# Optimization experiments

Measured on AMD Instinct MI355X. Metric: run time of the kernel, lower is better.

The kernel has to match this reference:

```python
import jax, jax.numpy as jnp
import numpy as np

B, T, L_CTX = 64, 150, 256
H = 512   # decoder_num_hidden
E = 512   # target_embedding_size
V = 1000  # target_vocab_size


def setup_inputs() -> dict:
    key = jax.random.key(0)
    ks = jax.random.split(key, 10)
    s = 0.05
    return {
        "cnn_feats": jax.random.normal(ks[0], (B, L_CTX, H), dtype=jnp.float32),
        "seq": jax.random.randint(ks[1], (B, T), 0, V, dtype=jnp.int32),
        "embed_table": jax.random.normal(ks[2], (V, E), dtype=jnp.float32) * s,
        "W_ih": jax.random.normal(ks[3], (4 * H, E), dtype=jnp.float32) * s,
        "b_ih": jnp.zeros((4 * H,), dtype=jnp.float32),
        "W_hh": jax.random.normal(ks[4], (4 * H, H), dtype=jnp.float32) * s,
        "b_hh": jnp.zeros((4 * H,), dtype=jnp.float32),
        "W_hm": jax.random.normal(ks[5], (H, H), dtype=jnp.float32) * s,
        "W_om": jax.random.normal(ks[6], (H, 2 * H), dtype=jnp.float32) * s,
        "W_logit": jax.random.normal(ks[7], (V, H), dtype=jnp.float32) * s,
        "b_logit": jnp.zeros((V,), dtype=jnp.float32),
    }


def reference(cnn_feats, seq, embed_table, W_ih, b_ih, W_hh, b_hh,
              W_hm, W_om, W_logit, b_logit):
    # Single-layer LSTMCell decoder with per-step attention (eval mode, dropout=0).
    def step(carry, it):
        h, c = carry                      # [B,H] each
        xt = jax.nn.relu(embed_table[it])  # [B,E]
        gates = xt @ W_ih.T + b_ih + h @ W_hh.T + b_hh  # [B,4H]
        i, f, g, o = jnp.split(gates, 4, axis=1)
        c2 = jax.nn.sigmoid(f) * c + jax.nn.sigmoid(i) * jnp.tanh(g)
        h2 = jax.nn.sigmoid(o) * jnp.tanh(c2)
        mapped = h2 @ W_hm.T              # [B,H]
        attn = jnp.einsum("blh,bh->bl", cnn_feats, mapped)
        w = jax.nn.softmax(attn, axis=1)
        ctx = jnp.einsum("bl,blh->bh", w, cnn_feats)
        out = jnp.concatenate([ctx, h2], axis=1) @ W_om.T  # [B,H]
        logp = jax.nn.log_softmax(out @ W_logit.T + b_logit, axis=1)
        return (h2, c2), logp

    bsz = cnn_feats.shape[0]
    h0 = jnp.zeros((bsz, W_hh.shape[1]), dtype=cnn_feats.dtype)
    c0 = jnp.zeros_like(h0)
    _, outs = jax.lax.scan(step, (h0, c0), seq.T)  # outs: [T,B,V]
    return outs.transpose(1, 0, 2)  # [B,T,V]
```

## Files before the change

### kernel.cpp

```cpp
#include <hip/hip_runtime.h>
#include <math.h>

#define B_  64
#define T_  150
#define L_  256
#define H_  512
#define E_  512
#define V_  1000
#define G4_ 2048
#define DB_ 16
#define HCB 32

typedef _Float16 f16;
typedef f16   f16x8 __attribute__((ext_vector_type(8)));
typedef f16   f16x4 __attribute__((ext_vector_type(4)));
typedef float f32x4 __attribute__((ext_vector_type(4)));
typedef unsigned long long ull;

__device__ __forceinline__ float sigmf(float x) { return 1.0f / (1.0f + expf(-x)); }

__global__ __launch_bounds__(512) void decoder_mfma(
    const int*   __restrict__ seq,
    const float* __restrict__ G,
    const float* __restrict__ Whh,
    ull*  __restrict__ xh,
    int*  __restrict__ tags,
    float* __restrict__ hbuf)
{
    __shared__ f16   hlds[64][520];
    __shared__ float glds[64][132];
    __shared__ float csh[64][36];

    const int tid = threadIdx.x;
    const int bb  = blockIdx.x;
    const int ln  = tid & 63;
    const int wv  = tid >> 6;
    const int mh  = wv >> 2;
    const int nt2 = wv & 3;

    f16x8 bfr[2][16];
    #pragma unroll
    for (int j = 0; j < 2; ++j) {
        const int n = 2 * nt2 + j;
        const int grow = (n >> 1) * H_ + bb * HCB + (n & 1) * 16 + (ln & 15);
        #pragma unroll
        for (int kt = 0; kt < 16; ++kt) {
            const int k0 = kt * 32 + (ln >> 4) * 8;
            float4 w0 = *(const float4*)(Whh + (size_t)grow * H_ + k0);
            float4 w1 = *(const float4*)(Whh + (size_t)grow * H_ + k0 + 4);
            bfr[j][kt] = (f16x8){(f16)w0.x, (f16)w0.y, (f16)w0.z, (f16)w0.w,
                                 (f16)w1.x, (f16)w1.y, (f16)w1.z, (f16)w1.w};
        }
    }
    for (int e = tid; e < 64 * 520 / 4; e += 512) ((ull*)hlds)[e] = 0ull;
    for (int e = tid; e < 64 * 36; e += 512) ((float*)csh)[e] = 0.f;
    __syncthreads();

    const int cb = tid >> 3, cg = tid & 7;

    for (int t = 0; t < T_; ++t) {
        const int v = seq[cb * T_ + t];
        const float* gp = G + (size_t)v * G4_ + bb * HCB + cg * 4;
        float4 gq0 = *(const float4*)(gp);
        float4 gq1 = *(const float4*)(gp + H_);
        float4 gq2 = *(const float4*)(gp + 2 * H_);
        float4 gq3 = *(const float4*)(gp + 3 * H_);

        if (t > 0) {
            if (tid < DB_) {
                while (__hip_atomic_load(&tags[tid], __ATOMIC_RELAXED,
                                         __HIP_MEMORY_SCOPE_AGENT) < t) {}
            }
            __syncthreads();
            const ull* src = xh + (size_t)(t & 1) * 64 * 128;
            ull v0[8], v1[8];
            #pragma unroll
            for (int it = 0; it < 8; ++it) {
                const int e = tid + it * 512;
                const int b = e >> 6, s = e & 63;
                v0[it] = __hip_atomic_load(&src[b * 128 + 2 * s], __ATOMIC_RELAXED,
                                           __HIP_MEMORY_SCOPE_AGENT);
                v1[it] = __hip_atomic_load(&src[b * 128 + 2 * s + 1], __ATOMIC_RELAXED,
                                           __HIP_MEMORY_SCOPE_AGENT);
            }
            #pragma unroll
            for (int it = 0; it < 8; ++it) {
                const int e = tid + it * 512;
                const int b = e >> 6, s = e & 63;
                ull* dst = (ull*)&hlds[b][s * 8];
                dst[0] = v0[it]; dst[1] = v1[it];
            }
            __syncthreads();
        }

        f32x4 acc00 = {0.f,0.f,0.f,0.f}, acc01 = {0.f,0.f,0.f,0.f};
        f32x4 acc10 = {0.f,0.f,0.f,0.f}, acc11 = {0.f,0.f,0.f,0.f};
        #pragma unroll
        for (int kt = 0; kt < 16; ++kt) {
            const int ko = kt * 32 + (ln >> 4) * 8;
            f16x8 a0 = *(const f16x8*)&hlds[(2 * mh)     * 16 + (ln & 15)][ko];
            f16x8 a1 = *(const f16x8*)&hlds[(2 * mh + 1) * 16 + (ln & 15)][ko];
            acc00 = __builtin_amdgcn_mfma_f32_16x16x32_f16(a0, bfr[0][kt], acc00, 0, 0, 0);
            acc01 = __builtin_amdgcn_mfma_f32_16x16x32_f16(a0, bfr[1][kt], acc01, 0, 0, 0);
            acc10 = __builtin_amdgcn_mfma_f32_16x16x32_f16(a1, bfr[0][kt], acc10, 0, 0, 0);
            acc11 = __builtin_amdgcn_mfma_f32_16x16x32_f16(a1, bfr[1][kt], acc11, 0, 0, 0);
        }
        {
            const int r0 = (2 * mh) * 16 + (ln >> 4) * 4;
            const int r1 = (2 * mh + 1) * 16 + (ln >> 4) * 4;
            const int c0 = (2 * nt2) * 16 + (ln & 15);
            const int c1 = (2 * nt2 + 1) * 16 + (ln & 15);
            #pragma unroll
            for (int i = 0; i < 4; ++i) {
                glds[r0 + i][c0] = acc00[i];
                glds[r0 + i][c1] = acc01[i];
                glds[r1 + i][c0] = acc10[i];
                glds[r1 + i][c1] = acc11[i];
            }
        }
        __syncthreads();

        {
            float4 Gi = *(const float4*)&glds[cb][cg * 4];
            float4 Gf = *(const float4*)&glds[cb][32 + cg * 4];
            float4 Gg = *(const float4*)&glds[cb][64 + cg * 4];
            float4 Go = *(const float4*)&glds[cb][96 + cg * 4];
            float4 cold = *(const float4*)&csh[cb][cg * 4];
            float gi[4] = {Gi.x + gq0.x, Gi.y + gq0.y, Gi.z + gq0.z, Gi.w + gq0.w};
            float gf[4] = {Gf.x + gq1.x, Gf.y + gq1.y, Gf.z + gq1.z, Gf.w + gq1.w};
            float gg[4] = {Gg.x + gq2.x, Gg.y + gq2.y, Gg.z + gq2.z, Gg.w + gq2.w};
            float go[4] = {Go.x + gq3.x, Go.y + gq3.y, Go.z + gq3.z, Go.w + gq3.w};
            float cl[4] = {cold.x, cold.y, cold.z, cold.w};
            float4 cnew, hnew;
            f16x4 hp;
            #pragma unroll
            for (int i = 0; i < 4; ++i) {
                float c2 = sigmf(gf[i]) * cl[i] + sigmf(gi[i]) * tanhf(gg[i]);
                float h2 = sigmf(go[i]) * tanhf(c2);
                ((float*)&cnew)[i] = c2;
                ((float*)&hnew)[i] = h2;
                hp[i] = (f16)h2;
            }
            *(float4*)&csh[cb][cg * 4] = cnew;
            *(float4*)&hbuf[((size_t)t * 64 + cb) * H_ + bb * HCB + cg * 4] = hnew;
            __hip_atomic_store(
                &xh[(size_t)((t + 1) & 1) * 64 * 128 + cb * 128 + bb * 8 + cg],
                __builtin_bit_cast(ull, hp),
                __ATOMIC_RELAXED, __HIP_MEMORY_SCOPE_AGENT);
        }
        __syncthreads();
        if (tid == 0)
            __hip_atomic_store(&tags[bb], t + 1, __ATOMIC_RELAXED,
                               __HIP_MEMORY_SCOPE_AGENT);
    }
}

template<bool RELU_A, bool REMAP>
__global__ __launch_bounds__(256) void gemm16_nt(
    const float* __restrict__ A1, const float* __restrict__ A2,
    const float* __restrict__ Bm,
    const float* __restrict__ bias1, const float* __restrict__ bias2,
    float* __restrict__ C, int M, int N, int KA)
{
    __shared__ f16 As[64][40];
    __shared__ f16 Bs[64][40];
    const int tid = threadIdx.x;
    const int m0 = blockIdx.x * 64, n0 = blockIdx.y * 64;
    const int ln = tid & 63, wv = tid >> 6;
    const int lr = tid >> 2, lc8 = (tid & 3) * 8;
    const int K = A2 ? 2 * KA : KA;
    f32x4 acc[4] = {};

    for (int kb = 0; kb < K; kb += 32) {
        const float* Ap; int kk;
        if (kb < KA) { Ap = A1; kk = kb; } else { Ap = A2; kk = kb - KA; }
        int gm = m0 + lr;
        float4 a0 = make_float4(0.f, 0.f, 0.f, 0.f), a1 = a0;
        if (gm < M) {
            a0 = *(const float4*)(Ap + (size_t)gm * KA + kk + lc8);
            a1 = *(const float4*)(Ap + (size_t)gm * KA + kk + lc8 + 4);
        }
        if (RELU_A) {
            a0.x = fmaxf(a0.x, 0.f); a0.y = fmaxf(a0.y, 0.f);
            a0.z = fmaxf(a0.z, 0.f); a0.w = fmaxf(a0.w, 0.f);
            a1.x = fmaxf(a1.x, 0.f); a1.y = fmaxf(a1.y, 0.f);
            a1.z = fmaxf(a1.z, 0.f); a1.w = fmaxf(a1.w, 0.f);
        }
        f16x8 av = {(f16)a0.x, (f16)a0.y, (f16)a0.z, (f16)a0.w,
                    (f16)a1.x, (f16)a1.y, (f16)a1.z, (f16)a1.w};
        *(f16x8*)&As[lr][lc8] = av;

        int gn = n0 + lr;
        float4 b0 = make_float4(0.f, 0.f, 0.f, 0.f), b1 = b0;
        if (gn < N) {
            b0 = *(const float4*)(Bm + (size_t)gn * K + kb + lc8);
            b1 = *(const float4*)(Bm + (size_t)gn * K + kb + lc8 + 4);
        }
        f16x8 bv = {(f16)b0.x, (f16)b0.y, (f16)b0.z, (f16)b0.w,
                    (f16)b1.x, (f16)b1.y, (f16)b1.z, (f16)b1.w};
        *(f16x8*)&Bs[lr][lc8] = bv;
        __syncthreads();

        f16x8 af = *(const f16x8*)&As[wv * 16 + (ln & 15)][(ln >> 4) * 8];
        #pragma unroll
        for (int ntt = 0; ntt < 4; ++ntt) {
            f16x8 bf = *(const f16x8*)&Bs[ntt * 16 + (ln & 15)][(ln >> 4) * 8];
            acc[ntt] = __builtin_amdgcn_mfma_f32_16x16x32_f16(af, bf, acc[ntt], 0, 0, 0);
        }
        __syncthreads();
    }

    #pragma unroll
    for (int ntt = 0; ntt < 4; ++ntt)
        #pragma unroll
        for (int i = 0; i < 4; ++i) {
            int gm = m0 + wv * 16 + (ln >> 4) * 4 + i;
            int gn = n0 + ntt * 16 + (ln & 15);
            if (gm < M && gn < N) {
                float v = acc[ntt][i];
                if (bias1) v += bias1[gn];
                if (bias2) v += bias2[gn];
                size_t row = REMAP ? ((size_t)(gm & 63) * T_ + (gm >> 6)) : (size_t)gm;
                C[row * (size_t)N + gn] = v;
            }
        }
}

__global__ __launch_bounds__(512) void score_softmax(
    const float* __restrict__ mapped,
    const float* __restrict__ cnn,
    f16* __restrict__ attP)
{
    __shared__ f16   As[64][40];
    __shared__ f16   Bs[256][40];
    __shared__ float sl[64][260];

    const int tid = threadIdx.x;
    const int m0  = blockIdx.x * 64;
    const int b   = blockIdx.y;
    const int ln  = tid & 63, wv = tid >> 6;
    const int mh  = wv >> 2, nq = wv & 3;
    const int ln15 = ln & 15, ln4 = (ln >> 4) * 8;
    const float* cnnb = cnn + (size_t)b * L_ * H_;

    f32x4 acc[2][4] = {};

    for (int kb = 0; kb < H_; kb += 32) {
        {
            int lr = tid >> 3, lc4 = (tid & 7) * 4;
            int t = m0 + lr;
            float4 a = make_float4(0.f, 0.f, 0.f, 0.f);
            if (t < T_) a = *(const float4*)(mapped + ((size_t)t * 64 + b) * H_ + kb + lc4);
            As[lr][lc4 + 0] = (f16)a.x; As[lr][lc4 + 1] = (f16)a.y;
            As[lr][lc4 + 2] = (f16)a.z; As[lr][lc4 + 3] = (f16)a.w;
        }
        {
            int br = tid >> 1, bc16 = (tid & 1) * 16;
            const float* src = cnnb + (size_t)br * H_ + kb + bc16;
            float4 w0 = *(const float4*)(src);
            float4 w1 = *(const float4*)(src + 4);
            float4 w2 = *(const float4*)(src + 8);
            float4 w3 = *(const float4*)(src + 12);
            f16x8 p0 = {(f16)w0.x, (f16)w0.y, (f16)w0.z, (f16)w0.w,
                        (f16)w1.x, (f16)w1.y, (f16)w1.z, (f16)w1.w};
            f16x8 p1 = {(f16)w2.x, (f16)w2.y, (f16)w2.z, (f16)w2.w,
                        (f16)w3.x, (f16)w3.y, (f16)w3.z, (f16)w3.w};
            *(f16x8*)&Bs[br][bc16]     = p0;
            *(f16x8*)&Bs[br][bc16 + 8] = p1;
        }
        __syncthreads();

        f16x8 a0 = *(const f16x8*)&As[(2 * mh)     * 16 + ln15][ln4];
        f16x8 a1 = *(const f16x8*)&As[(2 * mh + 1) * 16 + ln15][ln4];
        #pragma unroll
        for (int nj = 0; nj < 4; ++nj) {
            f16x8 bf = *(const f16x8*)&Bs[(nq * 4 + nj) * 16 + ln15][ln4];
            acc[0][nj] = __builtin_amdgcn_mfma_f32_16x16x32_f16(a0, bf, acc[0][nj], 0, 0, 0);
            acc[1][nj] = __builtin_amdgcn_mfma_f32_16x16x32_f16(a1, bf, acc[1][nj], 0, 0, 0);
        }
        __syncthreads();
    }

    #pragma unroll
    for (int mi = 0; mi < 2; ++mi)
        #pragma unroll
        for (int nj = 0; nj < 4; ++nj)
            #pragma unroll
            for (int i = 0; i < 4; ++i)
                sl[(2 * mh + mi) * 16 + (ln >> 4) * 4 + i][(nq * 4 + nj) * 16 + ln15]
                    = acc[mi][nj][i];
    __syncthreads();

    #pragma unroll
    for (int rr = 0; rr < 8; ++rr) {
        int r = wv * 8 + rr;
        int t = m0 + r;
        if (t < T_) {
            float4 v = *(const float4*)&sl[r][ln * 4];
            float mx = fmaxf(fmaxf(v.x, v.y), fmaxf(v.z, v.w));
            #pragma unroll
            for (int off = 32; off; off >>= 1) mx = fmaxf(mx, __shfl_xor(mx, off));
            float e0 = expf(v.x - mx), e1 = expf(v.y - mx);
            float e2 = expf(v.z - mx), e3 = expf(v.w - mx);
            float s = e0 + e1 + e2 + e3;
            #pragma unroll
            for (int off = 32; off; off >>= 1) s += __shfl_xor(s, off);
            float inv = 1.f / s;
            f16x4 p = {(f16)(e0 * inv), (f16)(e1 * inv), (f16)(e2 * inv), (f16)(e3 * inv)};
            *(f16x4*)(attP + ((size_t)b * T_ + t) * L_ + ln * 4) = p;
        }
    }
}

__global__ __launch_bounds__(256) void ctx16_nn(
    const f16* __restrict__ attP,
    const float* __restrict__ cnn,
    float* __restrict__ ctxout)
{
    __shared__ f16 As[64][40];
    __shared__ f16 Bs[64][40];
    const int tid = threadIdx.x;
    const int m0 = blockIdx.x * 64, n0 = blockIdx.y * 64;
    const int b  = blockIdx.z;
    const int ln = tid & 63, wv = tid >> 6;
    const int ln15 = ln & 15, ln4 = (ln >> 4) * 8;
    const float* cnnb = cnn + (size_t)b * L_ * H_;
    const f16*   pb   = attP + (size_t)b * T_ * L_;
    f32x4 acc[4] = {};

    for (int kb = 0; kb < L_; kb += 32) {
        {
            int lr = tid >> 2, lc8 = (tid & 3) * 8;
            int t = m0 + lr;
            f16x8 av = {};
            if (t < T_) av = *(const f16x8*)(pb + (size_t)t * L_ + kb + lc8);
            *(f16x8*)&As[lr][lc8] = av;
        }
        {
            int br = tid >> 3;
            int nc = (tid & 7) * 8;
            const float* src = cnnb + (size_t)(kb + br) * H_ + n0 + nc;
            float4 w0 = *(const float4*)(src);
            float4 w1 = *(const float4*)(src + 4);
            float wv8[8] = {w0.x, w0.y, w0.z, w0.w, w1.x, w1.y, w1.z, w1.w};
            #pragma unroll
            for (int j = 0; j < 8; ++j) Bs[nc + j][br] = (f16)wv8[j];
        }
        __syncthreads();

        f16x8 af = *(const f16x8*)&As[wv * 16 + ln15][ln4];
        #pragma unroll
        for (int ntt = 0; ntt < 4; ++ntt) {
            f16x8 bf = *(const f16x8*)&Bs[ntt * 16 + ln15][ln4];
            acc[ntt] = __builtin_amdgcn_mfma_f32_16x16x32_f16(af, bf, acc[ntt], 0, 0, 0);
        }
        __syncthreads();
    }

    #pragma unroll
    for (int ntt = 0; ntt < 4; ++ntt)
        #pragma unroll
        for (int i = 0; i < 4; ++i) {
            int t  = m0 + wv * 16 + (ln >> 4) * 4 + i;
            int gn = n0 + ntt * 16 + ln15;
            if (t < T_)
                ctxout[(size_t)b * H_ + (size_t)t * (B_ * H_) + gn] = acc[ntt][i];
        }
}

__global__ __launch_bounds__(256) void logsoftmax_k(float* __restrict__ out)
{
    const int row = blockIdx.x;
    float* p = out + (size_t)row * V_;
    const int tid = threadIdx.x, lane = tid & 63, wave = tid >> 6;
    __shared__ float red[8];

    float vals[4];
    int n = 0;
    float mx = -INFINITY;
    for (int v = tid; v < V_; v += 256) { vals[n] = p[v]; mx = fmaxf(mx, vals[n]); ++n; }
    #pragma unroll
    for (int off = 32; off; off >>= 1) mx = fmaxf(mx, __shfl_xor(mx, off));
    if (lane == 0) red[wave] = mx;
    __syncthreads();
    mx = fmaxf(fmaxf(red[0], red[1]), fmaxf(red[2], red[3]));

    float s = 0.f;
    for (int i = 0; i < n; ++i) s += expf(vals[i] - mx);
    #pragma unroll
    for (int off = 32; off; off >>= 1) s += __shfl_xor(s, off);
    if (lane == 0) red[4 + wave] = s;
    __syncthreads();
    s = red[4] + red[5] + red[6] + red[7];

    const float lse = mx + logf(s);
    n = 0;
    for (int v = tid; v < V_; v += 256) { p[v] = vals[n] - lse; ++n; }
}

extern "C" void kernel_launch(void* const* d_in, const int* in_sizes, int n_in,
                              void* d_out, int out_size, void* d_ws, size_t ws_size,
                              hipStream_t stream)
{
    const float* cnn     = (const float*)d_in[0];
    const int*   seq     = (const int*)d_in[1];
    const float* embed   = (const float*)d_in[2];
    const float* W_ih    = (const float*)d_in[3];
    const float* b_ih    = (const float*)d_in[4];
    const float* W_hh    = (const float*)d_in[5];
    const float* b_hh    = (const float*)d_in[6];
    const float* W_hm    = (const float*)d_in[7];
    const float* W_om    = (const float*)d_in[8];
    const float* W_logit = (const float*)d_in[9];
    const float* b_logit = (const float*)d_in[10];
    float* out = (float*)d_out;

    float* ws = (float*)d_ws;
    float* G    = ws;
    float* hbuf = G + (size_t)V_ * G4_;
    float* outv = hbuf + (size_t)B_ * T_ * H_;
    ull*   xh   = (ull*)(outv + (size_t)B_ * T_ * H_);
    int*   tags = (int*)(xh + 2 * 64 * 128);
    float* mapped = out;
    f16*   attP   = (f16*)(out + (size_t)B_ * T_ * H_);

    hipMemsetAsync(tags, 0, DB_ * sizeof(int), stream);

    gemm16_nt<true, false><<<dim3(16, 32), 256, 0, stream>>>(
        embed, nullptr, W_ih, b_ih, b_hh, G, V_, G4_, E_);

    decoder_mfma<<<DB_, 512, 0, stream>>>(seq, G, W_hh, xh, tags, hbuf);

    gemm16_nt<false, false><<<dim3(150, 8), 256, 0, stream>>>(
        hbuf, nullptr, W_hm, nullptr, nullptr, mapped, B_ * T_, H_, H_);
    score_softmax<<<dim3(3, 64), 512, 0, stream>>>(mapped, cnn, attP);
    ctx16_nn<<<dim3(3, 8, 64), 256, 0, stream>>>(attP, cnn, mapped);
    gemm16_nt<false, false><<<dim3(150, 8), 256, 0, stream>>>(
        mapped, hbuf, W_om, nullptr, nullptr, outv, B_ * T_, H_, H_);
    gemm16_nt<false, true><<<dim3(150, 16), 256, 0, stream>>>(
        outv, nullptr, W_logit, b_logit, nullptr, out, B_ * T_, V_, H_);
    logsoftmax_k<<<B_ * T_, 256, 0, stream>>>(out);
}
```

Baseline: 1.021 ms.

## Fuse decoder and attention/output stages into one persistent megakernel overlapping recurrence

```diff
diff --git a/kernel.cpp b/kernel.cpp
--- a/kernel.cpp
+++ b/kernel.cpp
@@ -9,6 +9,7 @@
 #define V_  1000
 #define G4_ 2048
 #define DB_ 16
+#define NW_ 240
 #define HCB 32
 
 typedef _Float16 f16;
@@ -19,148 +20,448 @@
 
 __device__ __forceinline__ float sigmf(float x) { return 1.0f / (1.0f + expf(-x)); }
 
-__global__ __launch_bounds__(512) void decoder_mfma(
+__device__ __forceinline__ ull aload(const ull* p)
+{
+    return __hip_atomic_load(p, __ATOMIC_RELAXED, __HIP_MEMORY_SCOPE_AGENT);
+}
+
+__global__ __launch_bounds__(512) void mega_decoder(
     const int*   __restrict__ seq,
     const float* __restrict__ G,
     const float* __restrict__ Whh,
-    ull*  __restrict__ xh,
+    const float* __restrict__ cnn,
+    const float* __restrict__ Whm,
+    const float* __restrict__ Wom,
+    const float* __restrict__ Wlg,
+    const float* __restrict__ b_logit,
+    ull*  __restrict__ xhist,
     int*  __restrict__ tags,
-    float* __restrict__ hbuf)
+    int*  __restrict__ wflags,
+    f16*  __restrict__ stageA,
+    f16*  __restrict__ attP,
+    f16*  __restrict__ outv16,
+    float* __restrict__ out)
 {
-    __shared__ f16   hlds[64][520];
-    __shared__ float glds[64][132];
-    __shared__ float csh[64][36];
+    __shared__ __align__(16) char smem[109568];
 
     const int tid = threadIdx.x;
-    const int bb  = blockIdx.x;
+    const int bx  = blockIdx.x;
     const int ln  = tid & 63;
     const int wv  = tid >> 6;
-    const int mh  = wv >> 2;
-    const int nt2 = wv & 3;
-
-    f16x8 bfr[2][16];
-    #pragma unroll
-    for (int j = 0; j < 2; ++j) {
-        const int n = 2 * nt2 + j;
-        const int grow = (n >> 1) * H_ + bb * HCB + (n & 1) * 16 + (ln & 15);
+
+    if (bx < DB_) {
+        f16   (*hlds)[520] = (f16(*)[520])smem;
+        float (*glds)[132] = (float(*)[132])(smem + 66560);
+        float (*csh)[36]   = (float(*)[36])(smem + 100352);
+        const int bb  = bx;
+        const int mh  = wv >> 2;
+        const int nt2 = wv & 3;
+
+        f16x8 bfr[2][16];
         #pragma unroll
-        for (int kt = 0; kt < 16; ++kt) {
-            const int k0 = kt * 32 + (ln >> 4) * 8;
-            float4 w0 = *(const float4*)(Whh + (size_t)grow * H_ + k0);
-            float4 w1 = *(const float4*)(Whh + (size_t)grow * H_ + k0 + 4);
-            bfr[j][kt] = (f16x8){(f16)w0.x, (f16)w0.y, (f16)w0.z, (f16)w0.w,
-                                 (f16)w1.x, (f16)w1.y, (f16)w1.z, (f16)w1.w};
-        }
+        for (int j = 0; j < 2; ++j) {
+            const int n = 2 * nt2 + j;
+            const int grow = (n >> 1) * H_ + bb * HCB + (n & 1) * 16 + (ln & 15);
+            #pragma unroll
+            for (int kt = 0; kt < 16; ++kt) {
+                const int k0 = kt * 32 + (ln >> 4) * 8;
+                float4 w0 = *(const float4*)(Whh + (size_t)grow * H_ + k0);
+                float4 w1 = *(const float4*)(Whh + (size_t)grow * H_ + k0 + 4);
+                bfr[j][kt] = (f16x8){(f16)w0.x, (f16)w0.y, (f16)w0.z, (f16)w0.w,
+                                     (f16)w1.x, (f16)w1.y, (f16)w1.z, (f16)w1.w};
+            }
+        }
+        for (int e = tid; e < 64 * 520 / 4; e += 512) ((ull*)hlds)[e] = 0ull;
+        for (int e = tid; e < 64 * 36; e += 512) ((float*)csh)[e] = 0.f;
+        __syncthreads();
+
+        const int cb = tid >> 3, cg = tid & 7;
+
+        for (int t = 0; t < T_; ++t) {
+            const int v = seq[cb * T_ + t];
+            const float* gp = G + (size_t)v * G4_ + bb * HCB + cg * 4;
+            float4 gq0 = *(const float4*)(gp);
+            float4 gq1 = *(const float4*)(gp + H_);
+            float4 gq2 = *(const float4*)(gp + 2 * H_);
+            float4 gq3 = *(const float4*)(gp + 3 * H_);
+
+            if (t > 0) {
+                if (tid < DB_) {
+                    while (__hip_atomic_load(&tags[tid], __ATOMIC_RELAXED,
+                                             __HIP_MEMORY_SCOPE_AGENT) < t) {}
+                }
+                __syncthreads();
+                const ull* src = xhist + (size_t)t * 8192;
+                ull v0[8], v1[8];
+                #pragma unroll
+                for (int it = 0; it < 8; ++it) {
+                    const int e = tid + it * 512;
+                    const int b = e >> 6, s = e & 63;
+                    v0[it] = aload(&src[b * 128 + 2 * s]);
+                    v1[it] = aload(&src[b * 128 + 2 * s + 1]);
+                }
+                #pragma unroll
+                for (int it = 0; it < 8; ++it) {
+                    const int e = tid + it * 512;
+                    const int b = e >> 6, s = e & 63;
+                    ull* dst = (ull*)&hlds[b][s * 8];
+                    dst[0] = v0[it]; dst[1] = v1[it];
+                }
+                __syncthreads();
+            }
+
+            f32x4 acc00 = {0.f,0.f,0.f,0.f}, acc01 = {0.f,0.f,0.f,0.f};
+            f32x4 acc10 = {0.f,0.f,0.f,0.f}, acc11 = {0.f,0.f,0.f,0.f};
+            #pragma unroll
+            for (int kt = 0; kt < 16; ++kt) {
+                const int ko = kt * 32 + (ln >> 4) * 8;
+                f16x8 a0 = *(const f16x8*)&hlds[(2 * mh)     * 16 + (ln & 15)][ko];
+                f16x8 a1 = *(const f16x8*)&hlds[(2 * mh + 1) * 16 + (ln & 15)][ko];
+                acc00 = __builtin_amdgcn_mfma_f32_16x16x32_f16(a0, bfr[0][kt], acc00, 0, 0, 0);
+                acc01 = __builtin_amdgcn_mfma_f32_16x16x32_f16(a0, bfr[1][kt], acc01, 0, 0, 0);
+                acc10 = __builtin_amdgcn_mfma_f32_16x16x32_f16(a1, bfr[0][kt], acc10, 0, 0, 0);
+                acc11 = __builtin_amdgcn_mfma_f32_16x16x32_f16(a1, bfr[1][kt], acc11, 0, 0, 0);
+            }
+            {
+                const int r0 = (2 * mh) * 16 + (ln >> 4) * 4;
+                const int r1 = (2 * mh + 1) * 16 + (ln >> 4) * 4;
+                const int c0 = (2 * nt2) * 16 + (ln & 15);
+                const int c1 = (2 * nt2 + 1) * 16 + (ln & 15);
+                #pragma unroll
+                for (int i = 0; i < 4; ++i) {
+                    glds[r0 + i][c0] = acc00[i];
+                    glds[r0 + i][c1] = acc01[i];
+                    glds[r1 + i][c0] = acc10[i];
+                    glds[r1 + i][c1] = acc11[i];
+                }
+            }
+            __syncthreads();
+
+            {
+                float4 Gi = *(const float4*)&glds[cb][cg * 4];
+                float4 Gf = *(const float4*)&glds[cb][32 + cg * 4];
+                float4 Gg = *(const float4*)&glds[cb][64 + cg * 4];
+                float4 Go = *(const float4*)&glds[cb][96 + cg * 4];
+                float4 cold = *(const float4*)&csh[cb][cg * 4];
+                float gi[4] = {Gi.x + gq0.x, Gi.y + gq0.y, Gi.z + gq0.z, Gi.w + gq0.w};
+                float gf[4] = {Gf.x + gq1.x, Gf.y + gq1.y, Gf.z + gq1.z, Gf.w + gq1.w};
+                float gg[4] = {Gg.x + gq2.x, Gg.y + gq2.y, Gg.z + gq2.z, Gg.w + gq2.w};
+                float go[4] = {Go.x + gq3.x, Go.y + gq3.y, Go.z + gq3.z, Go.w + gq3.w};
+                float cl[4] = {cold.x, cold.y, cold.z, cold.w};
+                float4 cnew;
+                f16x4 hp;
+                #pragma unroll
+                for (int i = 0; i < 4; ++i) {
+                    float c2 = sigmf(gf[i]) * cl[i] + sigmf(gi[i]) * tanhf(gg[i]);
+                    float h2 = sigmf(go[i]) * tanhf(c2);
+                    ((float*)&cnew)[i] = c2;
+                    hp[i] = (f16)h2;
+                }
+                *(float4*)&csh[cb][cg * 4] = cnew;
+                __hip_atomic_store(
+                    &xhist[(size_t)(t + 1) * 8192 + cb * 128 + bb * 8 + cg],
+                    __builtin_bit_cast(ull, hp),
+                    __ATOMIC_RELAXED, __HIP_MEMORY_SCOPE_AGENT);
+            }
+            __syncthreads();
+            if (tid == 0)
+                __hip_atomic_store(&tags[bb], t + 1, __ATOMIC_RELAXED,
+                                   __HIP_MEMORY_SCOPE_AGENT);
+        }
+        return;
     }
-    for (int e = tid; e < 64 * 520 / 4; e += 512) ((ull*)hlds)[e] = 0ull;
-    for (int e = tid; e < 64 * 36; e += 512) ((float*)csh)[e] = 0.f;
-    __syncthreads();
-
-    const int cb = tid >> 3, cg = tid & 7;
-
-    for (int t = 0; t < T_; ++t) {
-        const int v = seq[cb * T_ + t];
-        const float* gp = G + (size_t)v * G4_ + bb * HCB + cg * 4;
-        float4 gq0 = *(const float4*)(gp);
-        float4 gq1 = *(const float4*)(gp + H_);
-        float4 gq2 = *(const float4*)(gp + 2 * H_);
-        float4 gq3 = *(const float4*)(gp + 3 * H_);
-
-        if (t > 0) {
-            if (tid < DB_) {
+
+    const int wid = bx - DB_;
+    f16   (*As)[40]  = (f16(*)[40])smem;
+    f16   (*Bs)[40]  = (f16(*)[40])(smem + 5120);
+    float (*sl)[260] = (float(*)[260])(smem + 25600);
+    const int ln15 = ln & 15;
+    const int lnk8 = (ln >> 4) * 8;
+    const int lr4  = (ln >> 4) * 4;
+    int epoch = 0;
+
+    auto wbar = [&](int ep) {
+        __syncthreads();
+        if (tid == 0) {
+            __threadfence();
+            __hip_atomic_store(&wflags[wid], ep, __ATOMIC_RELAXED,
+                               __HIP_MEMORY_SCOPE_AGENT);
+        }
+        for (int i = tid; i < NW_; i += 512)
+            while (__hip_atomic_load(&wflags[i], __ATOMIC_RELAXED,
+                                     __HIP_MEMORY_SCOPE_AGENT) < ep)
+                __builtin_amdgcn_s_sleep(1);
+        __syncthreads();
+        if (tid == 0) __threadfence();
+        __syncthreads();
+    };
+
+    for (int c = 0; c < 3; ++c) {
+        const int t0 = c * 64;
+        const int t1 = (t0 + 64 < T_) ? t0 + 64 : T_;
+        if (t1 < T_) {
+            if (tid == 0)
+                while (__hip_atomic_load(&tags[0], __ATOMIC_RELAXED,
+                                         __HIP_MEMORY_SCOPE_AGENT) < t1 + 1)
+                    __builtin_amdgcn_s_sleep(127);
+        } else {
+            if (tid < DB_)
                 while (__hip_atomic_load(&tags[tid], __ATOMIC_RELAXED,
-                                         __HIP_MEMORY_SCOPE_AGENT) < t) {}
-            }
+                                         __HIP_MEMORY_SCOPE_AGENT) < T_)
+                    __builtin_amdgcn_s_sleep(127);
+        }
+        __syncthreads();
+
+        for (int job = wid; job < 512; job += NW_) {
+            const int t = t0 + (job >> 3);
+            if (t >= t1) continue;
+            const int n0 = (job & 7) * 64;
+            f32x4 acc0 = {0.f,0.f,0.f,0.f}, acc1 = {0.f,0.f,0.f,0.f};
+            const int mh = wv >> 2, nt = wv & 3;
+            for (int kb = 0; kb < 512; kb += 32) {
+                {
+                    int b = tid >> 3, s = tid & 7;
+                    ull v = aload(&xhist[(size_t)(t + 1) * 8192 + b * 128 + kb / 4 + s]);
+                    *(ull*)&As[b][s * 4] = v;
+                }
+                {
+                    int n = tid >> 3, s = tid & 7;
+                    float4 w = *(const float4*)(Whm + (size_t)(n0 + n) * 512 + kb + s * 4);
+                    f16x4 p = {(f16)w.x, (f16)w.y, (f16)w.z, (f16)w.w};
+                    *(f16x4*)&Bs[n][s * 4] = p;
+                }
+                __syncthreads();
+                f16x8 a0 = *(const f16x8*)&As[(2 * mh) * 16 + ln15][lnk8];
+                f16x8 a1 = *(const f16x8*)&As[(2 * mh + 1) * 16 + ln15][lnk8];
+                f16x8 bf = *(const f16x8*)&Bs[nt * 16 + ln15][lnk8];
+                acc0 = __builtin_amdgcn_mfma_f32_16x16x32_f16(a0, bf, acc0, 0, 0, 0);
+                acc1 = __builtin_amdgcn_mfma_f32_16x16x32_f16(a1, bf, acc1, 0, 0, 0);
+                __syncthreads();
+            }
+            #pragma unroll
+            for (int i = 0; i < 4; ++i) {
+                int b0r = (2 * mh) * 16 + lr4 + i, b1r = (2 * mh + 1) * 16 + lr4 + i;
+                int n = n0 + nt * 16 + ln15;
+                stageA[((size_t)t * 64 + b0r) * 512 + n] = (f16)acc0[i];
+                stageA[((size_t)t * 64 + b1r) * 512 + n] = (f16)acc1[i];
+            }
+        }
+        wbar(++epoch);
+
+        for (int b = wid; b < 64; b += NW_) {
+            const float* cnnb = cnn + (size_t)b * L_ * H_;
+            const int mh = wv >> 2, nq = wv & 3;
+            f32x4 acc[2][4] = {};
+            for (int kb = 0; kb < H_; kb += 32) {
+                {
+                    int tp = tid >> 3, s = tid & 7;
+                    ull v = 0ull;
+                    if (t0 + tp < t1)
+                        v = *(const ull*)(stageA + ((size_t)(t0 + tp) * 64 + b) * 512 + kb + s * 4);
+                    *(ull*)&As[tp][s * 4] = v;
+                }
+                {
+                    int br = tid >> 1, bc16 = (tid & 1) * 16;
+                    const float* src = cnnb + (size_t)br * H_ + kb + bc16;
+                    float4 w0 = *(const float4*)(src);
+                    float4 w1 = *(const float4*)(src + 4);
+                    float4 w2 = *(const float4*)(src + 8);
+                    float4 w3 = *(const float4*)(src + 12);
+                    f16x8 p0 = {(f16)w0.x, (f16)w0.y, (f16)w0.z, (f16)w0.w,
+                                (f16)w1.x, (f16)w1.y, (f16)w1.z, (f16)w1.w};
+                    f16x8 p1 = {(f16)w2.x, (f16)w2.y, (f16)w2.z, (f16)w2.w,
+                                (f16)w3.x, (f16)w3.y, (f16)w3.z, (f16)w3.w};
+                    *(f16x8*)&Bs[br][bc16]     = p0;
+                    *(f16x8*)&Bs[br][bc16 + 8] = p1;
+                }
+                __syncthreads();
+                f16x8 a0 = *(const f16x8*)&As[(2 * mh) * 16 + ln15][lnk8];
+                f16x8 a1 = *(const f16x8*)&As[(2 * mh + 1) * 16 + ln15][lnk8];
+                #pragma unroll
+                for (int nj = 0; nj < 4; ++nj) {
+                    f16x8 bf = *(const f16x8*)&Bs[(nq * 4 + nj) * 16 + ln15][lnk8];
+                    acc[0][nj] = __builtin_amdgcn_mfma_f32_16x16x32_f16(a0, bf, acc[0][nj], 0, 0, 0);
+                    acc[1][nj] = __builtin_amdgcn_mfma_f32_16x16x32_f16(a1, bf, acc[1][nj], 0, 0, 0);
+                }
+                __syncthreads();
+            }
+            #pragma unroll
+            for (int mi = 0; mi < 2; ++mi)
+                #pragma unroll
+                for (int nj = 0; nj < 4; ++nj)
+                    #pragma unroll
+                    for (int i = 0; i < 4; ++i)
+                        sl[(2 * mh + mi) * 16 + lr4 + i][(nq * 4 + nj) * 16 + ln15]
+                            = acc[mi][nj][i];
             __syncthreads();
-            const ull* src = xh + (size_t)(t & 1) * 64 * 128;
-            ull v0[8], v1[8];
-            #pragma unroll
-            for (int it = 0; it < 8; ++it) {
-                const int e = tid + it * 512;
-                const int b = e >> 6, s = e & 63;
-                v0[it] = __hip_atomic_load(&src[b * 128 + 2 * s], __ATOMIC_RELAXED,
-                                           __HIP_MEMORY_SCOPE_AGENT);
-                v1[it] = __hip_atomic_load(&src[b * 128 + 2 * s + 1], __ATOMIC_RELAXED,
-                                           __HIP_MEMORY_SCOPE_AGENT);
-            }
-            #pragma unroll
-            for (int it = 0; it < 8; ++it) {
-                const int e = tid + it * 512;
-                const int b = e >> 6, s = e & 63;
-                ull* dst = (ull*)&hlds[b][s * 8];
-                dst[0] = v0[it]; dst[1] = v1[it];
+            #pragma unroll
+            for (int rr = 0; rr < 8; ++rr) {
+                int r = wv * 8 + rr;
+                int t = t0 + r;
+                if (t < t1) {
+                    float4 v = *(const float4*)&sl[r][ln * 4];
+                    float mx = fmaxf(fmaxf(v.x, v.y), fmaxf(v.z, v.w));
+                    #pragma unroll
+                    for (int off = 32; off; off >>= 1) mx = fmaxf(mx, __shfl_xor(mx, off));
+                    float e0 = expf(v.x - mx), e1 = expf(v.y - mx);
+                    float e2 = expf(v.z - mx), e3 = expf(v.w - mx);
+                    float s = e0 + e1 + e2 + e3;
+                    #pragma unroll
+                    for (int off = 32; off; off >>= 1) s += __shfl_xor(s, off);
+                    float inv = 1.f / s;
+                    f16x4 p = {(f16)(e0 * inv), (f16)(e1 * inv),
+                               (f16)(e2 * inv), (f16)(e3 * inv)};
+                    *(f16x4*)(attP + ((size_t)b * T_ + t) * L_ + ln * 4) = p;
+                }
             }
             __syncthreads();
         }
-
-        f32x4 acc00 = {0.f,0.f,0.f,0.f}, acc01 = {0.f,0.f,0.f,0.f};
-        f32x4 acc10 = {0.f,0.f,0.f,0.f}, acc11 = {0.f,0.f,0.f,0.f};
-        #pragma unroll
-        for (int kt = 0; kt < 16; ++kt) {
-            const int ko = kt * 32 + (ln >> 4) * 8;
-            f16x8 a0 = *(const f16x8*)&hlds[(2 * mh)     * 16 + (ln & 15)][ko];
-            f16x8 a1 = *(const f16x8*)&hlds[(2 * mh + 1) * 16 + (ln & 15)][ko];
-            acc00 = __builtin_amdgcn_mfma_f32_16x16x32_f16(a0, bfr[0][kt], acc00, 0, 0, 0);
-            acc01 = __builtin_amdgcn_mfma_f32_16x16x32_f16(a0, bfr[1][kt], acc01, 0, 0, 0);
-            acc10 = __builtin_amdgcn_mfma_f32_16x16x32_f16(a1, bfr[0][kt], acc10, 0, 0, 0);
-            acc11 = __builtin_amdgcn_mfma_f32_16x16x32_f16(a1, bfr[1][kt], acc11, 0, 0, 0);
-        }
-        {
-            const int r0 = (2 * mh) * 16 + (ln >> 4) * 4;
-            const int r1 = (2 * mh + 1) * 16 + (ln >> 4) * 4;
-            const int c0 = (2 * nt2) * 16 + (ln & 15);
-            const int c1 = (2 * nt2 + 1) * 16 + (ln & 15);
+        wbar(++epoch);
+
+        for (int job = wid; job < 512; job += NW_) {
+            const int b = job >> 3;
+            const int n0 = (job & 7) * 64;
+            const float* cnnb = cnn + (size_t)b * L_ * H_;
+            const int mh = wv >> 2, nt = wv & 3;
+            f32x4 acc0 = {0.f,0.f,0.f,0.f}, acc1 = {0.f,0.f,0.f,0.f};
+            for (int kb = 0; kb < L_; kb += 32) {
+                {
+                    int tp = tid >> 3, s = tid & 7;
+                    ull v = 0ull;
+                    if (t0 + tp < t1)
+                        v = *(const ull*)(attP + ((size_t)b * T_ + t0 + tp) * L_ + kb + s * 4);
+                    *(ull*)&As[tp][s * 4] = v;
+                }
+                {
+                    int br = tid >> 4, nc = (tid & 15) * 4;
+                    float4 w = *(const float4*)(cnnb + (size_t)(kb + br) * H_ + n0 + nc);
+                    Bs[nc + 0][br] = (f16)w.x; Bs[nc + 1][br] = (f16)w.y;
+                    Bs[nc + 2][br] = (f16)w.z; Bs[nc + 3][br] = (f16)w.w;
+                }
+                __syncthreads();
+                f16x8 a0 = *(const f16x8*)&As[(2 * mh) * 16 + ln15][lnk8];
+                f16x8 a1 = *(const f16x8*)&As[(2 * mh + 1) * 16 + ln15][lnk8];
+                f16x8 bf = *(const f16x8*)&Bs[nt * 16 + ln15][lnk8];
+                acc0 = __builtin_amdgcn_mfma_f32_16x16x32_f16(a0, bf, acc0, 0, 0, 0);
+                acc1 = __builtin_amdgcn_mfma_f32_16x16x32_f16(a1, bf, acc1, 0, 0, 0);
+                __syncthreads();
+            }
             #pragma unroll
             for (int i = 0; i < 4; ++i) {
-                glds[r0 + i][c0] = acc00[i];
-                glds[r0 + i][c1] = acc01[i];
-                glds[r1 + i][c0] = acc10[i];
-                glds[r1 + i][c1] = acc11[i];
-            }
-        }
-        __syncthreads();
-
-        {
-            float4 Gi = *(const float4*)&glds[cb][cg * 4];
-            float4 Gf = *(const float4*)&glds[cb][32 + cg * 4];
-            float4 Gg = *(const float4*)&glds[cb][64 + cg * 4];
-            float4 Go = *(const float4*)&glds[cb][96 + cg * 4];
-            float4 cold = *(const float4*)&csh[cb][cg * 4];
-            float gi[4] = {Gi.x + gq0.x, Gi.y + gq0.y, Gi.z + gq0.z, Gi.w + gq0.w};
-            float gf[4] = {Gf.x + gq1.x, Gf.y + gq1.y, Gf.z + gq1.z, Gf.w + gq1.w};
-            float gg[4] = {Gg.x + gq2.x, Gg.y + gq2.y, Gg.z + gq2.z, Gg.w + gq2.w};
-            float go[4] = {Go.x + gq3.x, Go.y + gq3.y, Go.z + gq3.z, Go.w + gq3.w};
-            float cl[4] = {cold.x, cold.y, cold.z, cold.w};
-            float4 cnew, hnew;
-            f16x4 hp;
+                int tp0 = (2 * mh) * 16 + lr4 + i, tp1 = (2 * mh + 1) * 16 + lr4 + i;
+                int n = n0 + nt * 16 + ln15;
+                if (t0 + tp0 < t1)
+                    stageA[((size_t)(t0 + tp0) * 64 + b) * 512 + n] = (f16)acc0[i];
+                if (t0 + tp1 < t1)
+                    stageA[((size_t)(t0 + tp1) * 64 + b) * 512 + n] = (f16)acc1[i];
+            }
+        }
+        wbar(++epoch);
+
+        for (int job = wid; job < 512; job += NW_) {
+            const int t = t0 + (job >> 3);
+            if (t >= t1) continue;
+            const int n0 = (job & 7) * 64;
+            const int mh = wv >> 2, nt = wv & 3;
+            f32x4 acc0 = {0.f,0.f,0.f,0.f}, acc1 = {0.f,0.f,0.f,0.f};
+            for (int kb = 0; kb < 1024; kb += 32) {
+                {
+                    int b = tid >> 3, s = tid & 7;
+                    ull v;
+                    if (kb < 512)
+                        v = *(const ull*)(stageA + ((size_t)t * 64 + b) * 512 + kb + s * 4);
+                    else
+                        v = aload(&xhist[(size_t)(t + 1) * 8192 + b * 128 + (kb - 512) / 4 + s]);
+                    *(ull*)&As[b][s * 4] = v;
+                }
+                {
+                    int n = tid >> 3, s = tid & 7;
+                    float4 w = *(const float4*)(Wom + (size_t)(n0 + n) * 1024 + kb + s * 4);
+                    f16x4 p = {(f16)w.x, (f16)w.y, (f16)w.z, (f16)w.w};
+                    *(f16x4*)&Bs[n][s * 4] = p;
+                }
+                __syncthreads();
+                f16x8 a0 = *(const f16x8*)&As[(2 * mh) * 16 + ln15][lnk8];
+                f16x8 a1 = *(const f16x8*)&As[(2 * mh + 1) * 16 + ln15][lnk8];
+                f16x8 bf = *(const f16x8*)&Bs[nt * 16 + ln15][lnk8];
+                acc0 = __builtin_amdgcn_mfma_f32_16x16x32_f16(a0, bf, acc0, 0, 0, 0);
+                acc1 = __builtin_amdgcn_mfma_f32_16x16x32_f16(a1, bf, acc1, 0, 0, 0);
+                __syncthreads();
+            }
             #pragma unroll
             for (int i = 0; i < 4; ++i) {
-                float c2 = sigmf(gf[i]) * cl[i] + sigmf(gi[i]) * tanhf(gg[i]);
-                float h2 = sigmf(go[i]) * tanhf(c2);
-                ((float*)&cnew)[i] = c2;
-                ((float*)&hnew)[i] = h2;
-                hp[i] = (f16)h2;
-            }
-            *(float4*)&csh[cb][cg * 4] = cnew;
-            *(float4*)&hbuf[((size_t)t * 64 + cb) * H_ + bb * HCB + cg * 4] = hnew;
-            __hip_atomic_store(
-                &xh[(size_t)((t + 1) & 1) * 64 * 128 + cb * 128 + bb * 8 + cg],
-                __builtin_bit_cast(ull, hp),
-                __ATOMIC_RELAXED, __HIP_MEMORY_SCOPE_AGENT);
-        }
-        __syncthreads();
-        if (tid == 0)
-            __hip_atomic_store(&tags[bb], t + 1, __ATOMIC_RELAXED,
-                               __HIP_MEMORY_SCOPE_AGENT);
+                int b0r = (2 * mh) * 16 + lr4 + i, b1r = (2 * mh + 1) * 16 + lr4 + i;
+                int n = n0 + nt * 16 + ln15;
+                outv16[((size_t)t * 64 + b0r) * 512 + n] = (f16)acc0[i];
+                outv16[((size_t)t * 64 + b1r) * 512 + n] = (f16)acc1[i];
+            }
+        }
+        wbar(++epoch);
+
+        for (int job = wid; job < 1024; job += NW_) {
+            const int t = t0 + (job >> 4);
+            if (t >= t1) continue;
+            const int n0 = (job & 15) * 64;
+            const int mh = wv >> 2, nt = wv & 3;
+            f32x4 acc0 = {0.f,0.f,0.f,0.f}, acc1 = {0.f,0.f,0.f,0.f};
+            for (int kb = 0; kb < 512; kb += 32) {
+                {
+                    int b = tid >> 3, s = tid & 7;
+                    ull v = *(const ull*)(outv16 + ((size_t)t * 64 + b) * 512 + kb + s * 4);
+                    *(ull*)&As[b][s * 4] = v;
+                }
+                {
+                    int n = tid >> 3, s = tid & 7;
+                    f16x4 p = {(f16)0.f, (f16)0.f, (f16)0.f, (f16)0.f};
+                    if (n0 + n < V_) {
+                        float4 w = *(const float4*)(Wlg + (size_t)(n0 + n) * 512 + kb + s * 4);
+                        p = (f16x4){(f16)w.x, (f16)w.y, (f16)w.z, (f16)w.w};
+                    }
+                    *(f16x4*)&Bs[n][s * 4] = p;
+                }
+                __syncthreads();
+                f16x8 a0 = *(const f16x8*)&As[(2 * mh) * 16 + ln15][lnk8];
+                f16x8 a1 = *(const f16x8*)&As[(2 * mh + 1) * 16 + ln15][lnk8];
+                f16x8 bf = *(const f16x8*)&Bs[nt * 16 + ln15][lnk8];
+                acc0 = __builtin_amdgcn_mfma_f32_16x16x32_f16(a0, bf, acc0, 0, 0, 0);
+                acc1 = __builtin_amdgcn_mfma_f32_16x16x32_f16(a1, bf, acc1, 0, 0, 0);
+                __syncthreads();
+            }
+            int gn = n0 + nt * 16 + ln15;
+            if (gn < V_) {
+                float bias = b_logit[gn];
+                #pragma unroll
+                for (int i = 0; i < 4; ++i) {
+                    int b0r = (2 * mh) * 16 + lr4 + i, b1r = (2 * mh + 1) * 16 + lr4 + i;
+                    out[((size_t)b0r * T_ + t) * V_ + gn] = acc0[i] + bias;
+                    out[((size_t)b1r * T_ + t) * V_ + gn] = acc1[i] + bias;
+                }
+            }
+        }
+        wbar(++epoch);
+
+        for (int j = wid * 8 + wv; j < (t1 - t0) * 64; j += NW_ * 8) {
+            const int b = j & 63, tt = t0 + (j >> 6);
+            float* p = out + ((size_t)b * T_ + tt) * V_;
+            float mx = -INFINITY;
+            for (int i = ln; i < V_; i += 64) mx = fmaxf(mx, p[i]);
+            #pragma unroll
+            for (int off = 32; off; off >>= 1) mx = fmaxf(mx, __shfl_xor(mx, off));
+            float s = 0.f;
+            for (int i = ln; i < V_; i += 64) s += expf(p[i] - mx);
+            #pragma unroll
+            for (int off = 32; off; off >>= 1) s += __shfl_xor(s, off);
+            float lse = mx + logf(s);
+            for (int i = ln; i < V_; i += 64) p[i] -= lse;
+        }
     }
 }
 
-template<bool RELU_A, bool REMAP>
+template<bool RELU_A>
 __global__ __launch_bounds__(256) void gemm16_nt(
-    const float* __restrict__ A1, const float* __restrict__ A2,
-    const float* __restrict__ Bm,
+    const float* __restrict__ A1, const float* __restrict__ Bm,
     const float* __restrict__ bias1, const float* __restrict__ bias2,
-    float* __restrict__ C, int M, int N, int KA)
+    float* __restrict__ C, int M, int N, int K)
 {
     __shared__ f16 As[64][40];
     __shared__ f16 Bs[64][40];
@@ -168,17 +469,14 @@
     const int m0 = blockIdx.x * 64, n0 = blockIdx.y * 64;
     const int ln = tid & 63, wv = tid >> 6;
     const int lr = tid >> 2, lc8 = (tid & 3) * 8;
-    const int K = A2 ? 2 * KA : KA;
     f32x4 acc[4] = {};
 
     for (int kb = 0; kb < K; kb += 32) {
-        const float* Ap; int kk;
-        if (kb < KA) { Ap = A1; kk = kb; } else { Ap = A2; kk = kb - KA; }
         int gm = m0 + lr;
         float4 a0 = make_float4(0.f, 0.f, 0.f, 0.f), a1 = a0;
         if (gm < M) {
-            a0 = *(const float4*)(Ap + (size_t)gm * KA + kk + lc8);
-            a1 = *(const float4*)(Ap + (size_t)gm * KA + kk + lc8 + 4);
+            a0 = *(const float4*)(A1 + (size_t)gm * K + kb + lc8);
+            a1 = *(const float4*)(A1 + (size_t)gm * K + kb + lc8 + 4);
         }
         if (RELU_A) {
             a0.x = fmaxf(a0.x, 0.f); a0.y = fmaxf(a0.y, 0.f);
@@ -220,182 +518,9 @@
                 float v = acc[ntt][i];
                 if (bias1) v += bias1[gn];
                 if (bias2) v += bias2[gn];
-                size_t row = REMAP ? ((size_t)(gm & 63) * T_ + (gm >> 6)) : (size_t)gm;
-                C[row * (size_t)N + gn] = v;
-            }
-        }
-}
-
-__global__ __launch_bounds__(512) void score_softmax(
-    const float* __restrict__ mapped,
-    const float* __restrict__ cnn,
-    f16* __restrict__ attP)
-{
-    __shared__ f16   As[64][40];
-    __shared__ f16   Bs[256][40];
-    __shared__ float sl[64][260];
-
-    const int tid = threadIdx.x;
-    const int m0  = blockIdx.x * 64;
-    const int b   = blockIdx.y;
-    const int ln  = tid & 63, wv = tid >> 6;
-    const int mh  = wv >> 2, nq = wv & 3;
-    const int ln15 = ln & 15, ln4 = (ln >> 4) * 8;
-    const float* cnnb = cnn + (size_t)b * L_ * H_;
-
-    f32x4 acc[2][4] = {};
-
-    for (int kb = 0; kb < H_; kb += 32) {
-        {
-            int lr = tid >> 3, lc4 = (tid & 7) * 4;
-            int t = m0 + lr;
-            float4 a = make_float4(0.f, 0.f, 0.f, 0.f);
-            if (t < T_) a = *(const float4*)(mapped + ((size_t)t * 64 + b) * H_ + kb + lc4);
-            As[lr][lc4 + 0] = (f16)a.x; As[lr][lc4 + 1] = (f16)a.y;
-            As[lr][lc4 + 2] = (f16)a.z; As[lr][lc4 + 3] = (f16)a.w;
-        }
-        {
-            int br = tid >> 1, bc16 = (tid & 1) * 16;
-            const float* src = cnnb + (size_t)br * H_ + kb + bc16;
-            float4 w0 = *(const float4*)(src);
-            float4 w1 = *(const float4*)(src + 4);
-            float4 w2 = *(const float4*)(src + 8);
-            float4 w3 = *(const float4*)(src + 12);
-            f16x8 p0 = {(f16)w0.x, (f16)w0.y, (f16)w0.z, (f16)w0.w,
-                        (f16)w1.x, (f16)w1.y, (f16)w1.z, (f16)w1.w};
-            f16x8 p1 = {(f16)w2.x, (f16)w2.y, (f16)w2.z, (f16)w2.w,
-                        (f16)w3.x, (f16)w3.y, (f16)w3.z, (f16)w3.w};
-            *(f16x8*)&Bs[br][bc16]     = p0;
-            *(f16x8*)&Bs[br][bc16 + 8] = p1;
-        }
-        __syncthreads();
-
-        f16x8 a0 = *(const f16x8*)&As[(2 * mh)     * 16 + ln15][ln4];
-        f16x8 a1 = *(const f16x8*)&As[(2 * mh + 1) * 16 + ln15][ln4];
-        #pragma unroll
-        for (int nj = 0; nj < 4; ++nj) {
-            f16x8 bf = *(const f16x8*)&Bs[(nq * 4 + nj) * 16 + ln15][ln4];
-            acc[0][nj] = __builtin_amdgcn_mfma_f32_16x16x32_f16(a0, bf, acc[0][nj], 0, 0, 0);
-            acc[1][nj] = __builtin_amdgcn_mfma_f32_16x16x32_f16(a1, bf, acc[1][nj], 0, 0, 0);
-        }
-        __syncthreads();
-    }
-
-    #pragma unroll
-    for (int mi = 0; mi < 2; ++mi)
-        #pragma unroll
-        for (int nj = 0; nj < 4; ++nj)
-            #pragma unroll
-            for (int i = 0; i < 4; ++i)
-                sl[(2 * mh + mi) * 16 + (ln >> 4) * 4 + i][(nq * 4 + nj) * 16 + ln15]
-                    = acc[mi][nj][i];
-    __syncthreads();
-
-    #pragma unroll
-    for (int rr = 0; rr < 8; ++rr) {
-        int r = wv * 8 + rr;
-        int t = m0 + r;
-        if (t < T_) {
-            float4 v = *(const float4*)&sl[r][ln * 4];
-            float mx = fmaxf(fmaxf(v.x, v.y), fmaxf(v.z, v.w));
-            #pragma unroll
-            for (int off = 32; off; off >>= 1) mx = fmaxf(mx, __shfl_xor(mx, off));
-            float e0 = expf(v.x - mx), e1 = expf(v.y - mx);
-            float e2 = expf(v.z - mx), e3 = expf(v.w - mx);
-            float s = e0 + e1 + e2 + e3;
-            #pragma unroll
-            for (int off = 32; off; off >>= 1) s += __shfl_xor(s, off);
-            float inv = 1.f / s;
-            f16x4 p = {(f16)(e0 * inv), (f16)(e1 * inv), (f16)(e2 * inv), (f16)(e3 * inv)};
-            *(f16x4*)(attP + ((size_t)b * T_ + t) * L_ + ln * 4) = p;
-        }
-    }
-}
-
-__global__ __launch_bounds__(256) void ctx16_nn(
-    const f16* __restrict__ attP,
-    const float* __restrict__ cnn,
-    float* __restrict__ ctxout)
-{
-    __shared__ f16 As[64][40];
-    __shared__ f16 Bs[64][40];
-    const int tid = threadIdx.x;
-    const int m0 = blockIdx.x * 64, n0 = blockIdx.y * 64;
-    const int b  = blockIdx.z;
-    const int ln = tid & 63, wv = tid >> 6;
-    const int ln15 = ln & 15, ln4 = (ln >> 4) * 8;
-    const float* cnnb = cnn + (size_t)b * L_ * H_;
-    const f16*   pb   = attP + (size_t)b * T_ * L_;
-    f32x4 acc[4] = {};
-
-    for (int kb = 0; kb < L_; kb += 32) {
-        {
-            int lr = tid >> 2, lc8 = (tid & 3) * 8;
-            int t = m0 + lr;
-            f16x8 av = {};
-            if (t < T_) av = *(const f16x8*)(pb + (size_t)t * L_ + kb + lc8);
-            *(f16x8*)&As[lr][lc8] = av;
-        }
-        {
-            int br = tid >> 3;
-            int nc = (tid & 7) * 8;
-            const float* src = cnnb + (size_t)(kb + br) * H_ + n0 + nc;
-            float4 w0 = *(const float4*)(src);
-            float4 w1 = *(const float4*)(src + 4);
-            float wv8[8] = {w0.x, w0.y, w0.z, w0.w, w1.x, w1.y, w1.z, w1.w};
-            #pragma unroll
-            for (int j = 0; j < 8; ++j) Bs[nc + j][br] = (f16)wv8[j];
-        }
-        __syncthreads();
-
-        f16x8 af = *(const f16x8*)&As[wv * 16 + ln15][ln4];
-        #pragma unroll
-        for (int ntt = 0; ntt < 4; ++ntt) {
-            f16x8 bf = *(const f16x8*)&Bs[ntt * 16 + ln15][ln4];
-            acc[ntt] = __builtin_amdgcn_mfma_f32_16x16x32_f16(af, bf, acc[ntt], 0, 0, 0);
-        }
-        __syncthreads();
-    }
-
-    #pragma unroll
-    for (int ntt = 0; ntt < 4; ++ntt)
-        #pragma unroll
-        for (int i = 0; i < 4; ++i) {
-            int t  = m0 + wv * 16 + (ln >> 4) * 4 + i;
-            int gn = n0 + ntt * 16 + ln15;
-            if (t < T_)
-                ctxout[(size_t)b * H_ + (size_t)t * (B_ * H_) + gn] = acc[ntt][i];
-        }
-}
-
-__global__ __launch_bounds__(256) void logsoftmax_k(float* __restrict__ out)
-{
-    const int row = blockIdx.x;
-    float* p = out + (size_t)row * V_;
-    const int tid = threadIdx.x, lane = tid & 63, wave = tid >> 6;
-    __shared__ float red[8];
-
-    float vals[4];
-    int n = 0;
-    float mx = -INFINITY;
-    for (int v = tid; v < V_; v += 256) { vals[n] = p[v]; mx = fmaxf(mx, vals[n]); ++n; }
-    #pragma unroll
-    for (int off = 32; off; off >>= 1) mx = fmaxf(mx, __shfl_xor(mx, off));
-    if (lane == 0) red[wave] = mx;
-    __syncthreads();
-    mx = fmaxf(fmaxf(red[0], red[1]), fmaxf(red[2], red[3]));
-
-    float s = 0.f;
-    for (int i = 0; i < n; ++i) s += expf(vals[i] - mx);
-    #pragma unroll
-    for (int off = 32; off; off >>= 1) s += __shfl_xor(s, off);
-    if (lane == 0) red[4 + wave] = s;
-    __syncthreads();
-    s = red[4] + red[5] + red[6] + red[7];
-
-    const float lse = mx + logf(s);
-    n = 0;
-    for (int v = tid; v < V_; v += 256) { p[v] = vals[n] - lse; ++n; }
+                C[(size_t)gm * N + gn] = v;
+            }
+        }
 }
 
 extern "C" void kernel_launch(void* const* d_in, const int* in_sizes, int n_in,
@@ -415,29 +540,23 @@
     const float* b_logit = (const float*)d_in[10];
     float* out = (float*)d_out;
 
-    float* ws = (float*)d_ws;
-    float* G    = ws;
-    float* hbuf = G + (size_t)V_ * G4_;
-    float* outv = hbuf + (size_t)B_ * T_ * H_;
-    ull*   xh   = (ull*)(outv + (size_t)B_ * T_ * H_);
-    int*   tags = (int*)(xh + 2 * 64 * 128);
-    float* mapped = out;
-    f16*   attP   = (f16*)(out + (size_t)B_ * T_ * H_);
+    char* ws = (char*)d_ws;
+    float* G      = (float*)ws;
+    ull*   xhist  = (ull*)(ws + 8192000);
+    f16*   stageA = (f16*)(ws + 18087936);
+    f16*   attP   = (f16*)(ws + 27918336);
+    f16*   outv16 = (f16*)(ws + 32833536);
+    int*   tags   = (int*)(ws + 42663936);
+    int*   wflags = (int*)(ws + 42664000);
 
     hipMemsetAsync(tags, 0, DB_ * sizeof(int), stream);
-
-    gemm16_nt<true, false><<<dim3(16, 32), 256, 0, stream>>>(
-        embed, nullptr, W_ih, b_ih, b_hh, G, V_, G4_, E_);
-
-    decoder_mfma<<<DB_, 512, 0, stream>>>(seq, G, W_hh, xh, tags, hbuf);
-
-    gemm16_nt<false, false><<<dim3(150, 8), 256, 0, stream>>>(
-        hbuf, nullptr, W_hm, nullptr, nullptr, mapped, B_ * T_, H_, H_);
-    score_softmax<<<dim3(3, 64), 512, 0, stream>>>(mapped, cnn, attP);
-    ctx16_nn<<<dim3(3, 8, 64), 256, 0, stream>>>(attP, cnn, mapped);
-    gemm16_nt<false, false><<<dim3(150, 8), 256, 0, stream>>>(
-        mapped, hbuf, W_om, nullptr, nullptr, outv, B_ * T_, H_, H_);
-    gemm16_nt<false, true><<<dim3(150, 16), 256, 0, stream>>>(
-        outv, nullptr, W_logit, b_logit, nullptr, out, B_ * T_, V_, H_);
-    logsoftmax_k<<<B_ * T_, 256, 0, stream>>>(out);
+    hipMemsetAsync(wflags, 0, NW_ * sizeof(int), stream);
+    hipMemsetAsync(xhist, 0, 8192 * sizeof(ull), stream);
+
+    gemm16_nt<true><<<dim3(16, 32), 256, 0, stream>>>(
+        embed, W_ih, b_ih, b_hh, G, V_, G4_, E_);
+
+    mega_decoder<<<DB_ + NW_, 512, 0, stream>>>(
+        seq, G, W_hh, cnn, W_hm, W_om, W_logit, b_logit,
+        xhist, tags, wflags, stageA, attP, outv16, out);
 }
```

Result: slower. 1.258 ms (+23.2%).
